# Optimization experiments

Hardware: AMD Instinct MI355X
Metric: run time of the kernel (lower is better)

Reference implementation:

```python
import jax, jax.numpy as jnp
import numpy as np

DIM_IN, DIM, BS, H, W = 128, 64, 32, 64, 64
G, K = 5, 3          # KAN grid intervals and spline degree
EPS = 1e-5           # BatchNorm eps


def conv2d(x, w, b, groups=1, pad=0):
    # x: [B,C,H,W], w: [O, C//groups, kh, kw]
    y = jax.lax.conv_general_dilated(
        x, w, window_strides=(1, 1), padding=[(pad, pad), (pad, pad)],
        dimension_numbers=('NCHW', 'OIHW', 'NCHW'), feature_group_count=groups)
    return y + b[None, :, None, None]


def bn(x, g, b, m, v):
    # inference-mode BatchNorm2d
    inv = jax.lax.rsqrt(v + EPS)
    return g[None, :, None, None] * (x - m[None, :, None, None]) * inv[None, :, None, None] + b[None, :, None, None]


def make_grid():
    # extended knot vector over [-1,1], G intervals, degree K: G+2K+1 knots
    h = 2.0 / G
    t = jnp.arange(-K, G + K + 1, dtype=jnp.float32) * h - 1.0
    return jnp.broadcast_to(t, (DIM, G + 2 * K + 1))


def bspline_basis(x, t, k):
    # Cox-de Boor recursion. x: [N,in], t: [in, G+2k+1] -> B: [N,in,G+k]
    xe = x[..., None]
    B = ((xe >= t[:, :-1]) & (xe < t[:, 1:])).astype(x.dtype)
    for p in range(1, k + 1):
        B = ((xe - t[:, :-(p + 1)]) / (t[:, p:-1] - t[:, :-(p + 1)])) * B[..., :-1] \
          + ((t[:, p + 1:] - xe) / (t[:, p + 1:] - t[:, 1:-p])) * B[..., 1:]
    return B


def kan_forward(xk, coef, scale_base, scale_sp, kan_bias):
    # single KANLayer [dim -> dim]: silu residual branch + spline branch + node bias
    t = make_grid()
    B = bspline_basis(xk, t, K)                      # [N, in, G+K]
    y_base = jax.nn.silu(xk) @ scale_base            # [N, out]
    y_sp = jnp.einsum('nij,ioj->no', B, coef * scale_sp[:, :, None])
    return y_base + y_sp + kan_bias


def setup_inputs() -> dict:
    key = jax.random.key(0)
    ks = jax.random.split(key, 24)
    rn = lambda k, s, sc=0.05: jax.random.normal(k, s, jnp.float32) * sc
    return {
        'x': jax.random.normal(ks[0], (BS, DIM_IN, H, W), jnp.float32),
        'reduce_w': rn(ks[1], (DIM, DIM_IN, 1, 1), 0.1), 'reduce_b': rn(ks[2], (DIM,)),
        'dw_w': rn(ks[3], (DIM, 1, 7, 7), 0.1), 'dw_b': rn(ks[4], (DIM,)),
        'dw_g': 1.0 + rn(ks[5], (DIM,)), 'dw_beta': rn(ks[6], (DIM,)),
        'dw_m': rn(ks[7], (DIM,)), 'dw_v': 0.5 + jax.random.uniform(ks[8], (DIM,)),
        'f2_w': rn(ks[9], (DIM, DIM, 1, 1), 0.1), 'f2_b': rn(ks[10], (DIM,)),
        'coef': rn(ks[11], (DIM, DIM, G + K), 0.1),
        'scale_base': 1.0 / np.sqrt(DIM) + rn(ks[12], (DIM, DIM)),
        'scale_sp': 1.0 + rn(ks[13], (DIM, DIM)),
        'kan_bias': rn(ks[14], (DIM,)),
        'g_w': rn(ks[15], (DIM, DIM, 1, 1), 0.1), 'g_b': rn(ks[16], (DIM,)),
        'g_g': 1.0 + rn(ks[17], (DIM,)), 'g_beta': rn(ks[18], (DIM,)),
        'g_m': rn(ks[19], (DIM,)), 'g_v': 0.5 + jax.random.uniform(ks[20], (DIM,)),
        'dw2_w': rn(ks[21], (DIM, 1, 7, 7), 0.1), 'dw2_b': rn(ks[22], (DIM,)),
    }


def reference(x, reduce_w, reduce_b, dw_w, dw_b, dw_g, dw_beta, dw_m, dw_v,
              f2_w, f2_b, coef, scale_base, scale_sp, kan_bias,
              g_w, g_b, g_g, g_beta, g_m, g_v, dw2_w, dw2_b):
    x = conv2d(x, reduce_w, reduce_b)                       # dim_reduce 1x1
    inp = x
    xd = bn(conv2d(x, dw_w, dw_b, groups=DIM, pad=3), dw_g, dw_beta, dw_m, dw_v)  # 7x7 dwconv + BN
    bs, dim, h, w = xd.shape
    xk = xd.transpose(0, 2, 3, 1).reshape(bs * h * w, dim)  # tokenwise view
    x1 = kan_forward(xk, coef, scale_base, scale_sp, kan_bias)
    x1 = x1.reshape(bs, h, w, dim).transpose(0, 3, 1, 2)    # back to NCHW
    x2 = conv2d(xd, f2_w, f2_b)                             # f2 1x1
    y = x1 * x2                                             # elementwise gate
    y = bn(conv2d(y, g_w, g_b), g_g, g_beta, g_m, g_v)      # g 1x1 + BN
    y = conv2d(y, dw2_w, dw2_b, groups=DIM, pad=3)          # dwconv2 7x7
    return inp + y
```

## Files before the change

kernel.cpp:

```cpp
#include <hip/hip_runtime.h>
#include <hip/hip_bf16.h>

#define BSZ 32
#define CIN 128
#define CD 64
#define HH 64
#define WW 64
#define PLANE (HH * WW)
#define NPIX (BSZ * HH * WW)
#define NB 8
#define BN_EPS 1e-5f

typedef __attribute__((ext_vector_type(8))) short short8v;
typedef __attribute__((ext_vector_type(4))) float f32x4;
typedef __attribute__((ext_vector_type(4))) unsigned int u32x4;

static __device__ __forceinline__ short f2bf(float f) {
    __hip_bfloat16 h = __float2bfloat16(f);
    return __builtin_bit_cast(short, h);
}
static __device__ __forceinline__ unsigned int cvtpk(float lo, float hi) {
    unsigned int r;
    asm("v_cvt_pk_bf16_f32 %0, %1, %2" : "=v"(r) : "v"(lo), "v"(hi));
    return r;
}

__global__ __launch_bounds__(256) void k_prep(
    const float* __restrict__ coef, const float* __restrict__ ssp,
    const float* __restrict__ sb, const float* __restrict__ f2w,
    const float* __restrict__ reduce_w, const float* __restrict__ g_w,
    const float* __restrict__ dw_g, const float* __restrict__ dw_beta,
    const float* __restrict__ dw_m, const float* __restrict__ dw_v,
    const float* __restrict__ dw_b, const float* __restrict__ g_g,
    const float* __restrict__ g_beta, const float* __restrict__ g_m,
    const float* __restrict__ g_v, const float* __restrict__ g_b,
    short* __restrict__ W1f, short* __restrict__ W2f,
    short* __restrict__ WRf, short* __restrict__ WGf,
    float* __restrict__ cbuf)
{
    const int idx = blockIdx.x * 256 + threadIdx.x;
    if (idx < 36864) {
        const int e = idx & 7, l = (idx >> 3) & 63, c = (idx >> 9) & 3, s = idx >> 11;
        const int k = s * 32 + ((l >> 4) << 3) + e;
        const int j = (c << 4) + (l & 15);
        float v;
        if (k < 512) {
            const int i = k >> 3, t = k & 7;
            v = coef[(i * 64 + j) * 8 + t] * ssp[i * 64 + j];
        } else {
            v = sb[(k - 512) * 64 + j];
        }
        W1f[idx] = f2bf(v);
    } else if (idx < 45056) {
        const int f = idx - 36864;
        const int e = f & 7, l = (f >> 3) & 63, c = (f >> 9) & 3, s = f >> 11;
        const int k = s * 32 + ((l >> 4) << 3) + e;
        const int j = (c << 4) + (l & 15);
        W2f[f] = f2bf(f2w[j * 64 + k]);
    } else if (idx < 53248) {
        const int f = idx - 45056;
        const int e = f & 7, l = (f >> 3) & 63, c = (f >> 9) & 3, s = f >> 11;
        const int k = s * 32 + ((l >> 4) << 3) + e;
        const int j = (c << 4) + (l & 15);
        WRf[f] = f2bf(reduce_w[j * CIN + k]);
    } else if (idx < 57344) {
        const int f = idx - 53248;
        const int e = f & 7, l = (f >> 3) & 63, c = (f >> 9) & 3, s = f >> 11;
        const int k = s * 32 + ((l >> 4) << 3) + e;
        const int j = (c << 4) + (l & 15);
        WGf[f] = f2bf(g_w[j * 64 + k]);
    } else if (idx < 57600) {
        const int q = (idx - 57344) >> 6, c = idx & 63;
        if (q == 0) cbuf[c] = dw_g[c] * rsqrtf(dw_v[c] + BN_EPS);
        else if (q == 1) {
            float sc = dw_g[c] * rsqrtf(dw_v[c] + BN_EPS);
            cbuf[64 + c] = (dw_b[c] - dw_m[c]) * sc + dw_beta[c];
        } else if (q == 2) cbuf[128 + c] = g_g[c] * rsqrtf(g_v[c] + BN_EPS);
        else {
            float sc = g_g[c] * rsqrtf(g_v[c] + BN_EPS);
            cbuf[192 + c] = (g_b[c] - g_m[c]) * sc + g_beta[c];
        }
    }
}

__global__ __launch_bounds__(256) void k_reduce_mfma(
    const float* __restrict__ x, const short* __restrict__ WRf,
    const float* __restrict__ bias, float* __restrict__ out)
{
    __shared__ __align__(16) char smem[34048];
    short* As = (short*)smem;
    float* Osh = (float*)smem;
    const int bid = blockIdx.x;
    const int b = bid >> 5, h0 = (bid & 31) * 2;
    const int tid = threadIdx.x;
    const float* xb = x + (size_t)b * CIN * PLANE + h0 * WW;
#pragma unroll 1
    for (int p = 0; p < 64; ++p) {
        const int idx = tid + (p << 8);
        const int c = idx >> 7, rt = idx & 127;
        const float v = xb[(size_t)c * PLANE + rt];
        const int s = c >> 5, g = (c >> 3) & 3, e = c & 7;
        const int mt = rt >> 4, m = rt & 15;
        As[((mt * 4 + s) * 64 + (((g << 4) | m) ^ (s & 7))) * 8 + e] = f2bf(v);
    }
    __syncthreads();
    const int cw = tid >> 6, l = tid & 63;
    f32x4 acc[8];
#pragma unroll
    for (int i = 0; i < 8; ++i) acc[i] = (f32x4){0.f, 0.f, 0.f, 0.f};
#pragma unroll 1
    for (int s = 0; s < 4; ++s) {
        const short8v bfr = *(const short8v*)&WRf[((s * 4 + cw) * 64 + l) * 8];
        const int lx = l ^ (s & 7);
#pragma unroll
        for (int mt = 0; mt < 8; ++mt) {
            const short8v a = *(const short8v*)&As[((mt * 4 + s) * 64 + lx) * 8];
            acc[mt] = __builtin_amdgcn_mfma_f32_16x16x32_bf16(a, bfr, acc[mt], 0, 0, 0);
        }
    }
    __syncthreads();
    const int j = (cw << 4) + (l & 15);
    const float bj = bias[j];
    const int rb = (l >> 4) << 2;
#pragma unroll
    for (int mt = 0; mt < 8; ++mt)
#pragma unroll
        for (int r = 0; r < 4; ++r)
            Osh[j * 133 + mt * 16 + rb + r] = acc[mt][r] + bj;
    __syncthreads();
    float* ob = out + (size_t)b * CD * PLANE + h0 * WW;
#pragma unroll 1
    for (int p = 0; p < 32; ++p) {
        const int idx = tid + (p << 8);
        const int jj = idx >> 7, rt = idx & 127;
        ob[(size_t)jj * PLANE + rt] = Osh[jj * 133 + rt];
    }
}

template<bool RESID>
__global__ __launch_bounds__(256) void k_dwconv(
    const float* __restrict__ in, const float* __restrict__ filt,
    const float* __restrict__ sc, const float* __restrict__ shv,
    const float* __restrict__ resid, float* __restrict__ out)
{
    const int bid = blockIdx.x;
    const int b = bid >> 6, c4 = (bid >> 2) & 15, strip = bid & 3;
    const int H0 = strip << 4;
    const int c = c4 * 4 + (threadIdx.x >> 6);
    const int lane = threadIdx.x & 63;
    const size_t pbase = ((size_t)b * CD + c) * PLANE;
    const float* plane = in + pbase;
    const float* wp = filt + c * 49;
    float K[49];
#pragma unroll
    for (int q = 0; q < 49; ++q) K[q] = wp[q];
    const float scl = RESID ? 1.f : sc[c];
    const float shf = shv[c];
    const float* rplane = RESID ? (resid + pbase) : nullptr;
    float* oplane = out + pbase;

    float acc[7] = {0.f, 0.f, 0.f, 0.f, 0.f, 0.f, 0.f};
#pragma unroll
    for (int rr = 0; rr < 22; ++rr) {
        const int ra = H0 + rr - 3;
        float rowv = 0.f;
        if (ra >= 0 && ra < 64) rowv = plane[ra * 64 + lane];
        float sh[7];
        sh[3] = rowv;
#pragma unroll
        for (int d = 1; d <= 3; ++d) {
            float tp = __shfl(rowv, lane + d);
            sh[3 + d] = (lane + d < 64) ? tp : 0.f;
            float tm = __shfl(rowv, lane - d);
            sh[3 - d] = (lane - d >= 0) ? tm : 0.f;
        }
#pragma unroll
        for (int dy = 0; dy < 7; ++dy) {
            const int o = rr - dy;
            if (o >= 0 && o < 16) {
                const int slot = o % 7;
#pragma unroll
                for (int dx = 0; dx < 7; ++dx)
                    acc[slot] = fmaf(sh[dx], K[dy * 7 + dx], acc[slot]);
            }
        }
        const int done = rr - 6;
        if (done >= 0 && done < 16) {
            const int slot = done % 7;
            const int h = H0 + done;
            float val;
            if (RESID) val = acc[slot] + shf + rplane[h * 64 + lane];
            else       val = acc[slot] * scl + shf;
            oplane[h * 64 + lane] = val;
            acc[slot] = 0.f;
        }
    }
}

__global__ __launch_bounds__(256) void k_kan_fused(
    const float* __restrict__ xd, const short* __restrict__ W1f,
    const short* __restrict__ W2f, const short* __restrict__ WGf,
    const float* __restrict__ kb, const float* __restrict__ f2b,
    const float* __restrict__ gs, const float* __restrict__ gsh,
    float* __restrict__ z)
{
    __shared__ __align__(16) short As1[2 * 18 * 64 * 8];
    __shared__ __align__(16) short As2[2 * 2 * 64 * 8];
    const int tid = threadIdx.x;
    const int tg0 = blockIdx.x * 32;
    const int bb = tg0 >> 12, pix0 = tg0 & 4095;
    const float* xb = xd + (size_t)bb * CD * PLANE + pix0;
    const int tkn = tid & 31;
    const int w5 = tid >> 5;
    const int mt = tkn >> 4, m = tkn & 15;

    float vf[8], sf[8];
#pragma unroll
    for (int p = 0; p < 8; ++p) {
        const int c = w5 * 8 + p;
        const float v = xb[(size_t)c * PLANE + tkn];
        vf[p] = v;
        sf[p] = v * __builtin_amdgcn_rcpf(1.0f + __expf(-v));

        const float tt = (v + 2.2f) * 2.5f;
        const float fi = floorf(tt);
        const int i0 = (int)fi;
        const float u = tt - fi;
        const bool inr = (tt >= 0.0f) && (tt < 11.0f);
        const float u2 = u * u, u3 = u2 * u;
        const float t1 = 1.f - u;
        const float w0 = (1.f / 6.f) * t1 * t1 * t1;
        const float w3 = (1.f / 6.f) * u3;
        const float w1 = fmaf(0.5f, u3, 2.f / 3.f) - u2;
        const float w2 = 1.f - w0 - w1 - w3;
        const unsigned W01 = cvtpk(w0, w1);
        const unsigned W23 = cvtpk(w2, w3);
        const int q0 = i0 - 3;
        int a = q0 >> 1;
        const int bpar = q0 & 1;
        if (!inr) a = 100;
        const unsigned A1c = (W01 >> 16) | (W23 << 16);
        const unsigned C0 = bpar ? (W01 << 16) : W01;
        const unsigned C1 = bpar ? A1c : W23;
        const unsigned C2 = bpar ? (W23 >> 16) : 0u;
        u32x4 D;
        D.x = (a == 0) ? C0 : (a == -1) ? C1 : (a == -2) ? C2 : 0u;
        D.y = (a == 1) ? C0 : (a == 0) ? C1 : (a == -1) ? C2 : 0u;
        D.z = (a == 2) ? C0 : (a == 1) ? C1 : (a == 0) ? C2 : 0u;
        D.w = (a == 3) ? C0 : (a == 2) ? C1 : (a == 1) ? C2 : 0u;

        const int s = w5 * 2 + (p >> 2);
        const int phys = (((p & 3) << 4) | m) ^ (s & 7);
        *(u32x4*)&As1[((mt * 18 + s) * 64 + phys) * 8] = D;
    }
    {
        short8v vpk, spk;
#pragma unroll
        for (int q = 0; q < 4; ++q) {
            ((unsigned*)&vpk)[q] = cvtpk(vf[2 * q], vf[2 * q + 1]);
            ((unsigned*)&spk)[q] = cvtpk(sf[2 * q], sf[2 * q + 1]);
        }
        const int slot = ((w5 & 3) << 4) | m;
        const int s2 = 16 + (w5 >> 2);
        *(short8v*)&As1[((mt * 18 + s2) * 64 + (slot ^ (s2 & 7))) * 8] = spk;
        const int s3 = w5 >> 2;
        *(short8v*)&As2[((mt * 2 + s3) * 64 + (slot ^ (s3 & 7))) * 8] = vpk;
    }
    __syncthreads();

    const int cw = tid >> 6, l = tid & 63;
    f32x4 accA0 = {0.f,0.f,0.f,0.f}, accA1 = {0.f,0.f,0.f,0.f};
    f32x4 accB0 = {0.f,0.f,0.f,0.f}, accB1 = {0.f,0.f,0.f,0.f};
#pragma unroll 1
    for (int s = 0; s < 18; ++s) {
        const short8v bfr = *(const short8v*)&W1f[((s * 4 + cw) * 64 + l) * 8];
        const short8v a0 = *(const short8v*)&As1[((0 * 18 + s) * 64 + (l ^ (s & 7))) * 8];
        const short8v a1 = *(const short8v*)&As1[((1 * 18 + s) * 64 + (l ^ (s & 7))) * 8];
        accA0 = __builtin_amdgcn_mfma_f32_16x16x32_bf16(a0, bfr, accA0, 0, 0, 0);
        accA1 = __builtin_amdgcn_mfma_f32_16x16x32_bf16(a1, bfr, accA1, 0, 0, 0);
    }
#pragma unroll
    for (int s = 0; s < 2; ++s) {
        const short8v bfr = *(const short8v*)&W2f[((s * 4 + cw) * 64 + l) * 8];
        const short8v a0 = *(const short8v*)&As2[((0 * 2 + s) * 64 + (l ^ s)) * 8];
        const short8v a1 = *(const short8v*)&As2[((1 * 2 + s) * 64 + (l ^ s)) * 8];
        accB0 = __builtin_amdgcn_mfma_f32_16x16x32_bf16(a0, bfr, accB0, 0, 0, 0);
        accB1 = __builtin_amdgcn_mfma_f32_16x16x32_bf16(a1, bfr, accB1, 0, 0, 0);
    }

    const int j = (cw << 4) + (l & 15);
    const float kbj = kb[j], f2bj = f2b[j];
    const int rb = (l >> 4) << 2;
    float y0[4], y1[4];
#pragma unroll
    for (int r = 0; r < 4; ++r) {
        y0[r] = (accA0[r] + kbj) * (accB0[r] + f2bj);
        y1[r] = (accA1[r] + kbj) * (accB1[r] + f2bj);
    }
    __syncthreads();

    float* Ysh = (float*)As1;
#pragma unroll
    for (int r = 0; r < 4; ++r) {
        Ysh[j * 33 + rb + r]      = y0[r];
        Ysh[j * 33 + 16 + rb + r] = y1[r];
    }
    __syncthreads();

    {
        float yv[8];
#pragma unroll
        for (int p = 0; p < 8; ++p) yv[p] = Ysh[(w5 * 8 + p) * 33 + tkn];
        short8v ypk;
#pragma unroll
        for (int q = 0; q < 4; ++q)
            ((unsigned*)&ypk)[q] = cvtpk(yv[2 * q], yv[2 * q + 1]);
        const int slot = ((w5 & 3) << 4) | m;
        const int s3 = w5 >> 2;
        *(short8v*)&As2[((mt * 2 + s3) * 64 + (slot ^ (s3 & 7))) * 8] = ypk;
    }
    __syncthreads();

    f32x4 acc30 = {0.f,0.f,0.f,0.f}, acc31 = {0.f,0.f,0.f,0.f};
#pragma unroll
    for (int s = 0; s < 2; ++s) {
        const short8v bfr = *(const short8v*)&WGf[((s * 4 + cw) * 64 + l) * 8];
        const short8v a0 = *(const short8v*)&As2[((0 * 2 + s) * 64 + (l ^ s)) * 8];
        const short8v a1 = *(const short8v*)&As2[((1 * 2 + s) * 64 + (l ^ s)) * 8];
        acc30 = __builtin_amdgcn_mfma_f32_16x16x32_bf16(a0, bfr, acc30, 0, 0, 0);
        acc31 = __builtin_amdgcn_mfma_f32_16x16x32_bf16(a1, bfr, acc31, 0, 0, 0);
    }

    float* Osh = (float*)As1;
    const float sj = gs[j], hj = gsh[j];
#pragma unroll
    for (int r = 0; r < 4; ++r) {
        Osh[j * 33 + rb + r]      = acc30[r] * sj + hj;
        Osh[j * 33 + 16 + rb + r] = acc31[r] * sj + hj;
    }
    __syncthreads();
    float* zb = z + (size_t)bb * CD * PLANE + pix0;
#pragma unroll
    for (int q = 0; q < 8; ++q) {
        const int idx = tid + (q << 8);
        const int jj = idx >> 5, t2 = idx & 31;
        zb[(size_t)jj * PLANE + t2] = Osh[jj * 33 + t2];
    }
}

extern "C" void kernel_launch(void* const* d_in, const int* in_sizes, int n_in,
                              void* d_out, int out_size, void* d_ws, size_t ws_size,
                              hipStream_t stream)
{
    (void)in_sizes; (void)n_in; (void)out_size; (void)ws_size;
    const float* x        = (const float*)d_in[0];
    const float* reduce_w = (const float*)d_in[1];
    const float* reduce_b = (const float*)d_in[2];
    const float* dw_w     = (const float*)d_in[3];
    const float* dw_b     = (const float*)d_in[4];
    const float* dw_g     = (const float*)d_in[5];
    const float* dw_beta  = (const float*)d_in[6];
    const float* dw_m     = (const float*)d_in[7];
    const float* dw_v     = (const float*)d_in[8];
    const float* f2_w     = (const float*)d_in[9];
    const float* f2_b     = (const float*)d_in[10];
    const float* coef     = (const float*)d_in[11];
    const float* sbase    = (const float*)d_in[12];
    const float* ssp      = (const float*)d_in[13];
    const float* kbias    = (const float*)d_in[14];
    const float* g_w      = (const float*)d_in[15];
    const float* g_b      = (const float*)d_in[16];
    const float* g_g      = (const float*)d_in[17];
    const float* g_beta   = (const float*)d_in[18];
    const float* g_m      = (const float*)d_in[19];
    const float* g_v      = (const float*)d_in[20];
    const float* dw2_w    = (const float*)d_in[21];
    const float* dw2_b    = (const float*)d_in[22];
    float* out = (float*)d_out;

    const size_t NEL = (size_t)BSZ * CD * PLANE;
    short* W1f = (short*)d_ws;
    short* W2f = W1f + 36864;
    short* WRf = W2f + 8192;
    short* WGf = WRf + 8192;
    float* cbuf = (float*)((char*)d_ws + 115200);
    float* inp = (float*)((char*)d_ws + 131072);
    float* xdb = inp + NEL;
    float* z   = xdb + NEL;

    k_prep<<<225, 256, 0, stream>>>(coef, ssp, sbase, f2_w, reduce_w, g_w,
                                    dw_g, dw_beta, dw_m, dw_v, dw_b,
                                    g_g, g_beta, g_m, g_v, g_b,
                                    W1f, W2f, WRf, WGf, cbuf);
    k_reduce_mfma<<<BSZ * 32, 256, 0, stream>>>(x, WRf, reduce_b, inp);
    k_dwconv<false><<<BSZ * 16 * 4, 256, 0, stream>>>(inp, dw_w, cbuf, cbuf + 64, nullptr, xdb);
    k_kan_fused<<<NPIX / 32, 256, 0, stream>>>(xdb, W1f, W2f, WGf, kbias, f2_b,
                                               cbuf + 128, cbuf + 192, z);
    k_dwconv<true><<<BSZ * 16 * 4, 256, 0, stream>>>(z, dw2_w, nullptr, dw2_b, inp, out);
}
```

Before: 105.8 us.

## Cut shared-memory round trips and barriers in fused KAN epilogue

The intermediate gate product is now packed into bf16 pairs in a padded shared buffer, and the MFMA A-fragments for the g conv are gathered directly from it. This removes a separate fp32 transpose stage and two barriers. The final output is written straight from the MFMA accumulators as float4 stores instead of being staged through shared memory. The 18-step spline MFMA loop is fully unrolled and the per-channel constant loads are hoisted, at the cost of more registers, less coalesced global stores, and extra shared-memory usage.

```diff
diff --git a/kernel.cpp b/kernel.cpp
--- a/kernel.cpp
+++ b/kernel.cpp
@@ -23,6 +23,48 @@
     unsigned int r;
     asm("v_cvt_pk_bf16_f32 %0, %1, %2" : "=v"(r) : "v"(lo), "v"(hi));
     return r;
+}
+static __device__ __forceinline__ u32x4 basisD(float v) {
+    const float tt = (v + 2.2f) * 2.5f;
+    const float fi = floorf(tt);
+    const int i0 = (int)fi;
+    const float u = tt - fi;
+    const bool inr = (tt >= 0.0f) && (tt < 11.0f);
+    const float u2 = u * u, u3 = u2 * u;
+    const float t1 = 1.f - u;
+    const float w0 = (1.f / 6.f) * t1 * t1 * t1;
+    const float w3 = (1.f / 6.f) * u3;
+    const float w1 = fmaf(0.5f, u3, 2.f / 3.f) - u2;
+    const float w2 = 1.f - w0 - w1 - w3;
+    const unsigned W01 = cvtpk(w0, w1);
+    const unsigned W23 = cvtpk(w2, w3);
+    const int q0 = i0 - 3;
+    int a = q0 >> 1;
+    const int bpar = q0 & 1;
+    if (!inr) a = 100;
+    const unsigned A1c = (W01 >> 16) | (W23 << 16);
+    const unsigned C0 = bpar ? (W01 << 16) : W01;
+    const unsigned C1 = bpar ? A1c : W23;
+    const unsigned C2 = bpar ? (W23 >> 16) : 0u;
+    u32x4 D;
+    D.x = (a == 0) ? C0 : (a == -1) ? C1 : (a == -2) ? C2 : 0u;
+    D.y = (a == 1) ? C0 : (a == 0) ? C1 : (a == -1) ? C2 : 0u;
+    D.z = (a == 2) ? C0 : (a == 1) ? C1 : (a == 0) ? C2 : 0u;
+    D.w = (a == 3) ? C0 : (a == 2) ? C1 : (a == 1) ? C2 : 0u;
+    return D;
+}
+static __device__ __forceinline__ void gather_frags(
+    const unsigned* __restrict__ pad, int s3, int hi, int m,
+    short8v& f0, short8v& f1)
+{
+    unsigned q[8];
+#pragma unroll
+    for (int e = 0; e < 8; ++e) q[e] = pad[(s3 * 32 + 8 * hi + e) * 17 + m];
+#pragma unroll
+    for (int qi = 0; qi < 4; ++qi) {
+        ((unsigned*)&f0)[qi] = (q[2 * qi] & 0xffffu) | (q[2 * qi + 1] << 16);
+        ((unsigned*)&f1)[qi] = (q[2 * qi] >> 16) | (q[2 * qi + 1] & 0xffff0000u);
+    }
 }
 
 __global__ __launch_bounds__(256) void k_prep(
@@ -206,10 +248,12 @@
 {
     __shared__ __align__(16) short As1[2 * 18 * 64 * 8];
     __shared__ __align__(16) short As2[2 * 2 * 64 * 8];
+    __shared__ unsigned yPad[64 * 17];
     const int tid = threadIdx.x;
     const int tg0 = blockIdx.x * 32;
     const int bb = tg0 >> 12, pix0 = tg0 & 4095;
     const float* xb = xd + (size_t)bb * CD * PLANE + pix0;
+    float* zb = z + (size_t)bb * CD * PLANE + pix0;
     const int tkn = tid & 31;
     const int w5 = tid >> 5;
     const int mt = tkn >> 4, m = tkn & 15;
@@ -221,34 +265,7 @@
         const float v = xb[(size_t)c * PLANE + tkn];
         vf[p] = v;
         sf[p] = v * __builtin_amdgcn_rcpf(1.0f + __expf(-v));
-
-        const float tt = (v + 2.2f) * 2.5f;
-        const float fi = floorf(tt);
-        const int i0 = (int)fi;
-        const float u = tt - fi;
-        const bool inr = (tt >= 0.0f) && (tt < 11.0f);
-        const float u2 = u * u, u3 = u2 * u;
-        const float t1 = 1.f - u;
-        const float w0 = (1.f / 6.f) * t1 * t1 * t1;
-        const float w3 = (1.f / 6.f) * u3;
-        const float w1 = fmaf(0.5f, u3, 2.f / 3.f) - u2;
-        const float w2 = 1.f - w0 - w1 - w3;
-        const unsigned W01 = cvtpk(w0, w1);
-        const unsigned W23 = cvtpk(w2, w3);
-        const int q0 = i0 - 3;
-        int a = q0 >> 1;
-        const int bpar = q0 & 1;
-        if (!inr) a = 100;
-        const unsigned A1c = (W01 >> 16) | (W23 << 16);
-        const unsigned C0 = bpar ? (W01 << 16) : W01;
-        const unsigned C1 = bpar ? A1c : W23;
-        const unsigned C2 = bpar ? (W23 >> 16) : 0u;
-        u32x4 D;
-        D.x = (a == 0) ? C0 : (a == -1) ? C1 : (a == -2) ? C2 : 0u;
-        D.y = (a == 1) ? C0 : (a == 0) ? C1 : (a == -1) ? C2 : 0u;
-        D.z = (a == 2) ? C0 : (a == 1) ? C1 : (a == 0) ? C2 : 0u;
-        D.w = (a == 3) ? C0 : (a == 2) ? C1 : (a == 1) ? C2 : 0u;
-
+        const u32x4 D = basisD(v);
         const int s = w5 * 2 + (p >> 2);
         const int phys = (((p & 3) << 4) | m) ^ (s & 7);
         *(u32x4*)&As1[((mt * 18 + s) * 64 + phys) * 8] = D;
@@ -269,9 +286,16 @@
     __syncthreads();
 
     const int cw = tid >> 6, l = tid & 63;
+    const int hi = l >> 4;
+    const int j = (cw << 4) + (l & 15);
+    const int mq = l & 15;
+    const int rb = hi << 2;
+    const float kbj = kb[j], f2bj = f2b[j];
+    const float sj = gs[j], hj = gsh[j];
+
     f32x4 accA0 = {0.f,0.f,0.f,0.f}, accA1 = {0.f,0.f,0.f,0.f};
     f32x4 accB0 = {0.f,0.f,0.f,0.f}, accB1 = {0.f,0.f,0.f,0.f};
-#pragma unroll 1
+#pragma unroll
     for (int s = 0; s < 18; ++s) {
         const short8v bfr = *(const short8v*)&W1f[((s * 4 + cw) * 64 + l) * 8];
         const short8v a0 = *(const short8v*)&As1[((0 * 18 + s) * 64 + (l ^ (s & 7))) * 8];
@@ -288,64 +312,32 @@
         accB1 = __builtin_amdgcn_mfma_f32_16x16x32_bf16(a1, bfr, accB1, 0, 0, 0);
     }
 
-    const int j = (cw << 4) + (l & 15);
-    const float kbj = kb[j], f2bj = f2b[j];
-    const int rb = (l >> 4) << 2;
-    float y0[4], y1[4];
 #pragma unroll
     for (int r = 0; r < 4; ++r) {
-        y0[r] = (accA0[r] + kbj) * (accB0[r] + f2bj);
-        y1[r] = (accA1[r] + kbj) * (accB1[r] + f2bj);
-    }
-    __syncthreads();
-
-    float* Ysh = (float*)As1;
+        const float ya = (accA0[r] + kbj) * (accB0[r] + f2bj);
+        const float yb = (accA1[r] + kbj) * (accB1[r] + f2bj);
+        yPad[j * 17 + rb + r] = cvtpk(ya, yb);
+    }
+    __syncthreads();
+
+    f32x4 acc30 = {0.f,0.f,0.f,0.f}, acc31 = {0.f,0.f,0.f,0.f};
+#pragma unroll
+    for (int s3 = 0; s3 < 2; ++s3) {
+        const short8v bfr = *(const short8v*)&WGf[((s3 * 4 + cw) * 64 + l) * 8];
+        short8v f0, f1;
+        gather_frags(yPad, s3, hi, mq, f0, f1);
+        acc30 = __builtin_amdgcn_mfma_f32_16x16x32_bf16(f0, bfr, acc30, 0, 0, 0);
+        acc31 = __builtin_amdgcn_mfma_f32_16x16x32_bf16(f1, bfr, acc31, 0, 0, 0);
+    }
+
+    f32x4 o0, o1;
 #pragma unroll
     for (int r = 0; r < 4; ++r) {
-        Ysh[j * 33 + rb + r]      = y0[r];
-        Ysh[j * 33 + 16 + rb + r] = y1[r];
-    }
-    __syncthreads();
-
-    {
-        float yv[8];
-#pragma unroll
-        for (int p = 0; p < 8; ++p) yv[p] = Ysh[(w5 * 8 + p) * 33 + tkn];
-        short8v ypk;
-#pragma unroll
-        for (int q = 0; q < 4; ++q)
-            ((unsigned*)&ypk)[q] = cvtpk(yv[2 * q], yv[2 * q + 1]);
-        const int slot = ((w5 & 3) << 4) | m;
-        const int s3 = w5 >> 2;
-        *(short8v*)&As2[((mt * 2 + s3) * 64 + (slot ^ (s3 & 7))) * 8] = ypk;
-    }
-    __syncthreads();
-
-    f32x4 acc30 = {0.f,0.f,0.f,0.f}, acc31 = {0.f,0.f,0.f,0.f};
-#pragma unroll
-    for (int s = 0; s < 2; ++s) {
-        const short8v bfr = *(const short8v*)&WGf[((s * 4 + cw) * 64 + l) * 8];
-        const short8v a0 = *(const short8v*)&As2[((0 * 2 + s) * 64 + (l ^ s)) * 8];
-        const short8v a1 = *(const short8v*)&As2[((1 * 2 + s) * 64 + (l ^ s)) * 8];
-        acc30 = __builtin_amdgcn_mfma_f32_16x16x32_bf16(a0, bfr, acc30, 0, 0, 0);
-        acc31 = __builtin_amdgcn_mfma_f32_16x16x32_bf16(a1, bfr, acc31, 0, 0, 0);
-    }
-
-    float* Osh = (float*)As1;
-    const float sj = gs[j], hj = gsh[j];
-#pragma unroll
-    for (int r = 0; r < 4; ++r) {
-        Osh[j * 33 + rb + r]      = acc30[r] * sj + hj;
-        Osh[j * 33 + 16 + rb + r] = acc31[r] * sj + hj;
-    }
-    __syncthreads();
-    float* zb = z + (size_t)bb * CD * PLANE + pix0;
-#pragma unroll
-    for (int q = 0; q < 8; ++q) {
-        const int idx = tid + (q << 8);
-        const int jj = idx >> 5, t2 = idx & 31;
-        zb[(size_t)jj * PLANE + t2] = Osh[jj * 33 + t2];
-    }
+        o0[r] = acc30[r] * sj + hj;
+        o1[r] = acc31[r] * sj + hj;
+    }
+    *(f32x4*)&zb[(size_t)j * PLANE + rb] = o0;
+    *(f32x4*)&zb[(size_t)j * PLANE + 16 + rb] = o1;
 }
 
 extern "C" void kernel_launch(void* const* d_in, const int* in_sizes, int n_in,
```

Result: no change. 104.1 us (-1.6%).
